# Optimization experiments

Hardware: AMD Instinct MI355X
Metric: run time of the kernel (lower is better)

The kernel has to match this reference:

```python
import jax, jax.numpy as jnp
import numpy as np

DIM, HEADS, DIM_HEAD = 1024, 16, 64
DIM_INNER = HEADS * DIM_HEAD  # 1024
SCALE = DIM_HEAD ** -0.5


def _rope(t):
    # t: [b, h, n, d]; interleaved-pair RoPE (lucidrains rotary-embedding-torch default)
    d = t.shape[-1]
    n = t.shape[-2]
    inv_freq = 1.0 / (10000.0 ** (jnp.arange(0, d, 2, dtype=jnp.float32) / d))
    angles = jnp.arange(n, dtype=jnp.float32)[:, None] * inv_freq[None, :]  # [n, d/2]
    cos, sin = jnp.cos(angles), jnp.sin(angles)
    t1, t2 = t[..., 0::2], t[..., 1::2]
    r1 = t1 * cos - t2 * sin
    r2 = t1 * sin + t2 * cos
    return jnp.stack([r1, r2], axis=-1).reshape(t.shape)


def setup_inputs() -> dict:
    key = jax.random.key(0)
    ks = jax.random.split(key, 8)
    b, n = 2, 2048
    inp = {
        "x": jax.random.normal(ks[0], (b, n, DIM), dtype=jnp.float32),
        "value_residual": jax.random.normal(ks[1], (b, HEADS, n, DIM_HEAD), dtype=jnp.float32),
        "gamma": jnp.ones((DIM,), dtype=jnp.float32),
        "w_qkv": jax.random.normal(ks[2], (DIM, 3 * DIM_INNER), dtype=jnp.float32) * (DIM ** -0.5),
        "w_mix": jax.random.normal(ks[3], (DIM, HEADS), dtype=jnp.float32) * (DIM ** -0.5),
        "b_mix": jnp.zeros((HEADS,), dtype=jnp.float32),
        "w_gates": jax.random.normal(ks[4], (DIM, HEADS), dtype=jnp.float32) * (DIM ** -0.5),
        "b_gates": jnp.zeros((HEADS,), dtype=jnp.float32),
        "w_out": jax.random.normal(ks[5], (DIM_INNER, DIM), dtype=jnp.float32) * (DIM_INNER ** -0.5),
    }
    return inp


def reference(x, value_residual, gamma, w_qkv, w_mix, b_mix, w_gates, b_gates, w_out):
    b, n, _ = x.shape
    # RMSNorm (lucidrains style: F.normalize * sqrt(dim) * gamma)
    norm = jnp.sqrt(jnp.sum(x * x, axis=-1, keepdims=True))
    xn = x / jnp.maximum(norm, 1e-12) * (DIM ** 0.5) * gamma

    qkv = xn @ w_qkv  # [b, n, 3*h*d]
    qkv = qkv.reshape(b, n, 3, HEADS, DIM_HEAD)
    q, k, v = [jnp.transpose(qkv[:, :, i], (0, 2, 1, 3)) for i in range(3)]  # [b,h,n,d]
    original_values = v

    # learned value-residual lerp
    mix = jax.nn.sigmoid(xn @ w_mix + b_mix)            # [b, n, h]
    mix = jnp.transpose(mix, (0, 2, 1))[..., None]       # [b, h, n, 1]
    v = v * (1.0 - mix) + value_residual * mix

    # rotary on q, k
    q = _rope(q)
    k = _rope(k)

    scores = jnp.einsum("bhid,bhjd->bhij", q, k) * SCALE
    attn = jax.nn.softmax(scores, axis=-1)
    out = jnp.einsum("bhij,bhjd->bhid", attn, v)         # [b, h, n, d]

    gates = jax.nn.sigmoid(xn @ w_gates + b_gates)       # [b, n, h]
    out = out * jnp.transpose(gates, (0, 2, 1))[..., None]

    out = jnp.transpose(out, (0, 2, 1, 3)).reshape(b, n, DIM_INNER)
    return out @ w_out, original_values
```

## Files before the change

### kernel.cpp

```cpp
#include <hip/hip_runtime.h>
#include <hip/hip_bf16.h>
#include <math.h>

#define DIMSZ 1024
#define HEADS 16
#define DHEAD 64
#define NSEQ  2048
#define BATCH 2
#define ROWS  (BATCH*NSEQ)
#define SCALE 0.125f
#define LOG2E 1.4426950408889634f

typedef __attribute__((ext_vector_type(8))) short short8;
typedef __attribute__((ext_vector_type(4))) float floatx4;
typedef __attribute__((ext_vector_type(16))) float floatx16;
typedef __attribute__((ext_vector_type(4))) unsigned uintx4;

#define MFMA16(a,b,c) __builtin_amdgcn_mfma_f32_16x16x32_bf16(a,b,c,0,0,0)
#define MFMA32(a,b,c) __builtin_amdgcn_mfma_f32_32x32x16_bf16(a,b,c,0,0,0)

__device__ __forceinline__ void gl2lds16(const void* g, void* l) {
    __builtin_amdgcn_global_load_lds(
        (const __attribute__((address_space(1))) unsigned int*)g,
        (__attribute__((address_space(3))) unsigned int*)l, 16, 0, 0);
}

__device__ __forceinline__ unsigned short bf16r(float a) {
    unsigned u = __float_as_uint(a);
    u += 0x7fff + ((u >> 16) & 1);
    return (unsigned short)(u >> 16);
}
__device__ __forceinline__ unsigned pack_bf16(float a, float b) {
    unsigned ua = __float_as_uint(a), ub = __float_as_uint(b);
    ua += 0x7fff + ((ua >> 16) & 1);
    ub += 0x7fff + ((ub >> 16) & 1);
    return (ua >> 16) | (ub & 0xffff0000u);
}
__device__ __forceinline__ float2 bf2f(unsigned u) {
    float2 r;
    r.x = __uint_as_float(u << 16);
    r.y = __uint_as_float(u & 0xffff0000u);
    return r;
}
__device__ __forceinline__ unsigned cvtpk(float lo, float hi) {
    unsigned r;
    asm("v_cvt_pk_bf16_f32 %0, %1, %2" : "=v"(r) : "v"(lo), "v"(hi));
    return r;
}
__device__ __forceinline__ void pl32swap(unsigned &a, unsigned &b) {
#if __has_builtin(__builtin_amdgcn_permlane32_swap)
    auto r = __builtin_amdgcn_permlane32_swap(a, b, false, false);
    a = (unsigned)r[0]; b = (unsigned)r[1];
#else
    asm volatile("v_permlane32_swap_b32 %0, %1" : "+v"(a), "+v"(b));
#endif
}
__device__ __forceinline__ float fexp2(float x) {
#if __has_builtin(__builtin_amdgcn_exp2f)
    return __builtin_amdgcn_exp2f(x);
#else
    return exp2f(x);
#endif
}
__device__ __forceinline__ float fsin_rev(float x) {
#if __has_builtin(__builtin_amdgcn_sinf)
    return __builtin_amdgcn_sinf(x);
#else
    return __sinf(x * 6.28318530717958647692f);
#endif
}
__device__ __forceinline__ float fcos_rev(float x) {
#if __has_builtin(__builtin_amdgcn_cosf)
    return __builtin_amdgcn_cosf(x);
#else
    return __cosf(x * 6.28318530717958647692f);
#endif
}

__global__ __launch_bounds__(256) void transpose_all_kernel(
    const float* __restrict__ w_qkv, const float* __restrict__ w_out,
    const float* __restrict__ w_mix, const float* __restrict__ w_gates,
    unsigned short* __restrict__ wqkvT, unsigned short* __restrict__ woutT,
    unsigned short* __restrict__ wmgT)
{
    __shared__ float t[32][33];
    const int tx = threadIdx.x & 31, tyy = threadIdx.x >> 5;
    const int bx = blockIdx.x;
    const int k0 = blockIdx.y * 32;
    if (bx < 128) {
        const float* src;
        unsigned short* dst;
        int N, n0;
        if (bx < 96) { src = w_qkv; dst = wqkvT; N = 3*DIMSZ; n0 = bx*32; }
        else         { src = w_out; dst = woutT; N = DIMSZ;   n0 = (bx-96)*32; }
        #pragma unroll
        for (int i = 0; i < 4; i++)
            t[tyy*4 + i][tx] = src[(size_t)(k0 + tyy*4 + i)*N + n0 + tx];
        __syncthreads();
        #pragma unroll
        for (int i = 0; i < 4; i++)
            dst[(size_t)(n0 + tyy*4 + i)*DIMSZ + k0 + tx] = bf16r(t[tx][tyy*4 + i]);
    } else {
        #pragma unroll
        for (int i = 0; i < 4; i++) {
            const int kk = k0 + tyy*4 + i;
            t[tyy*4 + i][tx] = (tx < 16) ? w_mix[kk*16 + tx]
                                         : w_gates[kk*16 + (tx - 16)];
        }
        __syncthreads();
        #pragma unroll
        for (int i = 0; i < 4; i++)
            wmgT[(size_t)(tyy*4 + i)*DIMSZ + k0 + tx] = bf16r(t[tx][tyy*4 + i]);
    }
}

__global__ __launch_bounds__(256) void rmsnorm_kernel(
    const float* __restrict__ x, const float* __restrict__ gamma,
    unsigned short* __restrict__ xnb)
{
    const int row = blockIdx.x;
    const int tid = threadIdx.x;
    __shared__ float wred[4];

    const float4 xv = ((const float4*)(x + (size_t)row * DIMSZ))[tid];
    float ss = xv.x*xv.x + xv.y*xv.y + xv.z*xv.z + xv.w*xv.w;
    #pragma unroll
    for (int off = 1; off < 64; off <<= 1) ss += __shfl_xor(ss, off);
    if ((tid & 63) == 0) wred[tid >> 6] = ss;
    __syncthreads();
    const float total = wred[0] + wred[1] + wred[2] + wred[3];
    const float inv = 32.0f / fmaxf(sqrtf(total), 1e-12f);
    const float4 gv = ((const float4*)gamma)[tid];
    uint2 pk;
    pk.x = pack_bf16(xv.x * inv * gv.x, xv.y * inv * gv.y);
    pk.y = pack_bf16(xv.z * inv * gv.z, xv.w * inv * gv.w);
    ((uint2*)(xnb + (size_t)row * DIMSZ))[tid] = pk;
}

__global__ __launch_bounds__(256) void mix_gates_mfma(
    const unsigned short* __restrict__ A, const unsigned short* __restrict__ WG,
    const float* __restrict__ b_mix, const float* __restrict__ b_gates,
    float* __restrict__ mixo, float* __restrict__ gateso)
{
    __shared__ short As[128*32];
    __shared__ short Bs[32*32];
    const int tid = threadIdx.x;
    const int wv = tid >> 6, lane = tid & 63;
    const int g = lane >> 4, c = lane & 15;
    const int bm = blockIdx.x * 128;

    floatx4 acc[2][2];
    #pragma unroll
    for (int mt = 0; mt < 2; mt++)
        #pragma unroll
        for (int nt = 0; nt < 2; nt++) acc[mt][nt] = (floatx4){0.f,0.f,0.f,0.f};

    for (int k0 = 0; k0 < DIMSZ; k0 += 32) {
        __syncthreads();
        #pragma unroll
        for (int r = 0; r < 2; r++) {
            const int ch = tid + 256*r;
            const int row = ch >> 2, cc = ch & 3;
            gl2lds16(A + (size_t)(bm + row)*DIMSZ + k0 + cc*8, (void*)(As + ch*8));
        }
        if (tid < 128)
            gl2lds16(WG + (size_t)(tid >> 2)*DIMSZ + k0 + (tid & 3)*8, (void*)(Bs + tid*8));
        __syncthreads();
        short8 af[2], bf[2];
        #pragma unroll
        for (int mt = 0; mt < 2; mt++) af[mt] = *(const short8*)(As + (wv*32 + mt*16 + c)*32 + g*8);
        #pragma unroll
        for (int nt = 0; nt < 2; nt++) bf[nt] = *(const short8*)(Bs + (nt*16 + c)*32 + g*8);
        #pragma unroll
        for (int mt = 0; mt < 2; mt++)
            #pragma unroll
            for (int nt = 0; nt < 2; nt++)
                acc[mt][nt] = MFMA16(af[mt], bf[nt], acc[mt][nt]);
    }
    const float bm_c = b_mix[c], bg_c = b_gates[c];
    #pragma unroll
    for (int mt = 0; mt < 2; mt++)
        #pragma unroll
        for (int r2 = 0; r2 < 4; r2++) {
            const int row = bm + wv*32 + mt*16 + g*4 + r2;
            const float lm = acc[mt][0][r2] + bm_c;
            const float lg = acc[mt][1][r2] + bg_c;
            mixo[(size_t)row*HEADS + c]   = 1.0f / (1.0f + fexp2(-lm * LOG2E));
            gateso[(size_t)row*HEADS + c] = 1.0f / (1.0f + fexp2(-lg * LOG2E));
        }
}

__global__ __launch_bounds__(256) void gemm_qkv_mfma(
    const unsigned short* __restrict__ A, const unsigned short* __restrict__ BT,
    unsigned short* __restrict__ qb, unsigned short* __restrict__ kb,
    float* __restrict__ vb)
{
    __shared__ short As[2][128*32];
    __shared__ short Bs[2][128*32];
    const int tid = threadIdx.x;
    const int wv = tid >> 6, lane = tid & 63;
    const int g = lane >> 4, c = lane & 15;
    const int wm = wv >> 1, wn = wv & 1;

    const int id = blockIdx.y * gridDim.x + blockIdx.x;
    const int xcd = id & 7, j = id >> 3;
    const int bnb = (xcd & 1)*12 + (j % 12);
    const int byb = (xcd >> 1)*8 + (j / 12);
    const int bm = byb * 128, bn = bnb * 128;

    floatx4 acc[4][4];
    #pragma unroll
    for (int mt = 0; mt < 4; mt++)
        #pragma unroll
        for (int nt = 0; nt < 4; nt++) acc[mt][nt] = (floatx4){0.f,0.f,0.f,0.f};

    const int srow = tid >> 2, scc = tid & 3;
    #pragma unroll
    for (int r = 0; r < 2; r++) {
        const int ch = tid + 256*r;
        const int row = ch >> 2, cc = ch & 3;
        gl2lds16(A  + (size_t)(bm + row)*DIMSZ + cc*8, (void*)(&As[0][0] + ch*8));
        gl2lds16(BT + (size_t)(bn + row)*DIMSZ + cc*8, (void*)(&Bs[0][0] + ch*8));
    }
    __syncthreads();

    for (int k0 = 0; k0 < DIMSZ; k0 += 32) {
        const int cur = (k0 >> 5) & 1;
        if (k0 + 32 < DIMSZ) {
            #pragma unroll
            for (int r = 0; r < 2; r++) {
                const int ch = tid + 256*r;
                const int row = ch >> 2, cc = ch & 3;
                gl2lds16(A  + (size_t)(bm + row)*DIMSZ + k0 + 32 + cc*8, (void*)(&As[cur^1][0] + ch*8));
                gl2lds16(BT + (size_t)(bn + row)*DIMSZ + k0 + 32 + cc*8, (void*)(&Bs[cur^1][0] + ch*8));
            }
        }
        short8 af[4], bf[4];
        #pragma unroll
        for (int mt = 0; mt < 4; mt++) af[mt] = *(const short8*)(&As[cur][0] + (wm*64 + mt*16 + c)*32 + g*8);
        #pragma unroll
        for (int nt = 0; nt < 4; nt++) bf[nt] = *(const short8*)(&Bs[cur][0] + (wn*64 + nt*16 + c)*32 + g*8);
        __builtin_amdgcn_s_setprio(1);
        #pragma unroll
        for (int mt = 0; mt < 4; mt++)
            #pragma unroll
            for (int nt = 0; nt < 4; nt++)
                acc[mt][nt] = MFMA16(af[mt], bf[nt], acc[mt][nt]);
        __builtin_amdgcn_s_setprio(0);
        __syncthreads();
    }
    (void)srow; (void)scc;

    const int i3 = bn >> 10;
    const int nb = bn - (i3 << 10);
    if (i3 < 2) {
        unsigned short* dst = (i3 == 0) ? qb : kb;
        short* wbuf = &As[0][0] + wv*1152;
        const int rd_row = lane >> 2, seg = lane & 3;
        #pragma unroll
        for (int mt = 0; mt < 4; mt++) {
            #pragma unroll
            for (int nt = 0; nt < 4; nt++)
                #pragma unroll
                for (int r2 = 0; r2 < 4; r2++)
                    wbuf[(g*4 + r2)*72 + nt*16 + c] = (short)bf16r(acc[mt][nt][r2]);
            __builtin_amdgcn_s_waitcnt(0xc07f);
            const uint4 v0 = *(const uint4*)&wbuf[rd_row*72 + seg*16];
            const uint4 v1 = *(const uint4*)&wbuf[rd_row*72 + seg*16 + 8];
            const int row = bm + wm*64 + mt*16 + rd_row;
            const int col = nb + wn*64 + seg*16;
            const int hh = col >> 6, dd = col & 63;
            const int bb2 = row >> 11, pos = row & 2047;
            unsigned short* dp = dst + (((size_t)(bb2*HEADS + hh)*NSEQ) + pos)*DHEAD + dd;
            *(uint4*)dp = v0;
            *(uint4*)(dp + 8) = v1;
            __builtin_amdgcn_s_waitcnt(0xc07f);
        }
    } else {
        #pragma unroll
        for (int mt = 0; mt < 4; mt++)
            #pragma unroll
            for (int nt = 0; nt < 4; nt++)
                #pragma unroll
                for (int r2 = 0; r2 < 4; r2++) {
                    const int row = bm + wm*64 + mt*16 + g*4 + r2;
                    const int col = nb + wn*64 + nt*16 + c;
                    const int hh = col >> 6, dd = col & 63;
                    const int bb2 = row >> 11, pos = row & 2047;
                    vb[(((size_t)(bb2*HEADS + hh)*NSEQ) + pos)*DHEAD + dd] = acc[mt][nt][r2];
                }
    }
}

__global__ __launch_bounds__(256) void rope_blend_kernel2(
    unsigned short* __restrict__ q, unsigned short* __restrict__ k,
    const float* __restrict__ vorig, const float* __restrict__ vres,
    const float* __restrict__ mixb, unsigned short* __restrict__ vT)
{
    __shared__ unsigned short vt[64*72];
    const int tid = threadIdx.x;
    const int bh = blockIdx.y, bb = bh >> 4, h = bh & 15;
    const int p0 = blockIdx.x * 64;
    {
        const int pr = tid >> 2, d0 = (tid & 3) * 16;
        const int pos = p0 + pr;
        const size_t base = ((size_t)bh*NSEQ + pos)*DHEAD + d0;

        uint4 qr0 = *(uint4*)(q + base), qr1 = *(uint4*)(q + base + 8);
        uint4 kr0 = *(uint4*)(k + base), kr1 = *(uint4*)(k + base + 8);
        unsigned qw[8] = {qr0.x, qr0.y, qr0.z, qr0.w, qr1.x, qr1.y, qr1.z, qr1.w};
        unsigned kw[8] = {kr0.x, kr0.y, kr0.z, kr0.w, kr1.x, kr1.y, kr1.z, kr1.w};
        const float QSC = SCALE * LOG2E;
        const float posf = (float)pos;
        #pragma unroll
        for (int j = 0; j < 8; j++) {
            const float pf = (float)((d0 >> 1) + j);
            const float rev = posf * fexp2(-pf * 0.41524101186092029f
                                           - 2.6514961294723187f);
            const float rf = rev - floorf(rev);
            const float sn = fsin_rev(rf);
            const float cs = fcos_rev(rf);
            float2 qv = bf2f(qw[j]);
            float2 kv = bf2f(kw[j]);
            const float q1 = qv.x*cs - qv.y*sn, q2 = qv.x*sn + qv.y*cs;
            const float k1 = kv.x*cs - kv.y*sn, k2 = kv.x*sn + kv.y*cs;
            qw[j] = pack_bf16(q1*QSC, q2*QSC);
            kw[j] = pack_bf16(k1, k2);
        }
        *(uint4*)(q + base)     = *(uint4*)(qw + 0);
        *(uint4*)(q + base + 8) = *(uint4*)(qw + 4);
        *(uint4*)(k + base)     = *(uint4*)(kw + 0);
        *(uint4*)(k + base + 8) = *(uint4*)(kw + 4);

        float vv[16], vr[16];
        #pragma unroll
        for (int i = 0; i < 4; i++) {
            *(float4*)(vv + i*4) = *(const float4*)(vorig + base + i*4);
            *(float4*)(vr + i*4) = *(const float4*)(vres + base + i*4);
        }
        const float mx = mixb[((size_t)(bb*NSEQ + pos))*HEADS + h];
        #pragma unroll
        for (int j = 0; j < 8; j++) {
            const float b0 = vv[2*j]*(1.f-mx)   + vr[2*j]*mx;
            const float b1 = vv[2*j+1]*(1.f-mx) + vr[2*j+1]*mx;
            vt[pr*72 + d0 + 2*j]     = bf16r(b0);
            vt[pr*72 + d0 + 2*j + 1] = bf16r(b1);
        }
    }
    __syncthreads();
    {
        const int dd = tid >> 2, c0 = (tid & 3) * 16;
        unsigned o[8];
        #pragma unroll
        for (int j = 0; j < 8; j++) {
            const unsigned a  = vt[(c0 + 2*j)*72 + dd];
            const unsigned b2 = vt[(c0 + 2*j + 1)*72 + dd];
            o[j] = a | (b2 << 16);
        }
        unsigned short* dst = vT + ((size_t)bh*DHEAD + dd)*NSEQ + p0 + c0;
        *(uint4*)(dst)     = *(uint4*)(o + 0);
        *(uint4*)(dst + 8) = *(uint4*)(o + 4);
    }
}

__global__ __launch_bounds__(256, 4) void attn_mfma_kernel(
    const unsigned short* __restrict__ qg,
    const unsigned short* __restrict__ kg,
    const unsigned short* __restrict__ vT,
    unsigned short* __restrict__ Op0,
    unsigned short* __restrict__ Op1,
    float* __restrict__ lpart)
{
    __shared__ short Kt[2][64*64];
    __shared__ short Vt[2][64*64];

    const int tid = threadIdx.x;
    const int w = tid >> 6, lane = tid & 63;
    const int hi = lane >> 5, cq = lane & 31;

    int wg = blockIdx.y * gridDim.x + blockIdx.x;
    wg = (wg & 7) * 128 + (wg >> 3);
    const int q0 = (wg & 15) * 128;
    const int byy = wg >> 4;
    const int bh = byy >> 1, s = byy & 1;
    const int bb = bh >> 4, h = bh & 15;

    short8 qf[4];
    #pragma unroll
    for (int kd = 0; kd < 4; kd++)
        qf[kd] = *(const short8*)(qg + ((size_t)bh*NSEQ + q0 + w*32 + cq)*DHEAD + kd*16 + hi*8);

    floatx16 O0{}, O1{};
    float lsum = 0.f;

    const unsigned short* kbase = kg + (size_t)bh*NSEQ*DHEAD;
    const unsigned short* vbase = vT + (size_t)bh*DHEAD*NSEQ;

    {
        const int kt = s*16;
        #pragma unroll
        for (int r = 0; r < 2; r++) {
            const int ch = tid + 256*r;
            const int row = ch >> 3;
            const int u = (ch & 7) ^ (row & 7);
            gl2lds16(kbase + (size_t)(kt*64 + row)*DHEAD + u*8, (void*)(&Kt[0][0] + ch*8));
            gl2lds16(vbase + (size_t)row*NSEQ + kt*64 + u*8,   (void*)(&Vt[0][0] + ch*8));
        }
    }
    __syncthreads();

    for (int i = 0; i < 16; i++) {
        const int cur = i & 1;
        const short* Ktc = &Kt[cur][0];
        const short* Vtc = &Vt[cur][0];

        if (i < 15) {
            const int kt = s*16 + i + 1;
            short* Ktn = &Kt[cur ^ 1][0];
            short* Vtn = &Vt[cur ^ 1][0];
            #pragma unroll
            for (int r = 0; r < 2; r++) {
                const int ch = tid + 256*r;
                const int row = ch >> 3;
                const int u = (ch & 7) ^ (row & 7);
                gl2lds16(kbase + (size_t)(kt*64 + row)*DHEAD + u*8, (void*)(Ktn + ch*8));
                gl2lds16(vbase + (size_t)row*NSEQ + kt*64 + u*8,   (void*)(Vtn + ch*8));
            }
        }

        #pragma unroll
        for (int kt2 = 0; kt2 < 2; kt2++) {
            floatx16 accS{};
            const int rowk = kt2*32 + cq;
            __builtin_amdgcn_s_setprio(1);
            #pragma unroll
            for (int kd = 0; kd < 4; kd++) {
                short8 kf = *(const short8*)(Ktc + rowk*64 + (((kd*2 + hi) ^ (cq & 7)) * 8));
                accS = MFMA32(kf, qf[kd], accS);
            }
            __builtin_amdgcn_s_setprio(0);

            float p[16];
            #pragma unroll
            for (int r = 0; r < 16; r++) p[r] = fexp2(accS[r]);
            const float a1 = (p[0]+p[1]) + (p[2]+p[3]);
            const float a2 = (p[4]+p[5]) + (p[6]+p[7]);
            const float a3 = (p[8]+p[9]) + (p[10]+p[11]);
            const float a4 = (p[12]+p[13]) + (p[14]+p[15]);
            lsum += (a1+a2) + (a3+a4);

            unsigned d0 = cvtpk(p[0],  p[1]);
            unsigned d1 = cvtpk(p[2],  p[3]);
            unsigned d2 = cvtpk(p[4],  p[5]);
            unsigned d3 = cvtpk(p[6],  p[7]);
            unsigned d4 = cvtpk(p[8],  p[9]);
            unsigned d5 = cvtpk(p[10], p[11]);
            unsigned d6 = cvtpk(p[12], p[13]);
            unsigned d7 = cvtpk(p[14], p[15]);
            pl32swap(d0, d2);
            pl32swap(d1, d3);
            pl32swap(d4, d6);
            pl32swap(d5, d7);
            const uintx4 t0 = {d0, d1, d2, d3};
            const uintx4 t1 = {d4, d5, d6, d7};
            const short8 pf0 = __builtin_bit_cast(short8, t0);
            const short8 pf1 = __builtin_bit_cast(short8, t1);

            __builtin_amdgcn_s_setprio(1);
            #pragma unroll
            for (int ks2 = 0; ks2 < 2; ks2++) {
                const short8 pf = ks2 ? pf1 : pf0;
                #pragma unroll
                for (int nt2 = 0; nt2 < 2; nt2++) {
                    const int rv = nt2*32 + cq;
                    short8 vf = *(const short8*)(Vtc + rv*64 + (((kt2*4 + ks2*2 + hi) ^ (cq & 7)) * 8));
                    if (nt2 == 0) O0 = MFMA32(pf, vf, O0);
                    else          O1 = MFMA32(pf, vf, O1);
                }
            }
            __builtin_amdgcn_s_setprio(0);
        }
        __syncthreads();
    }

    unsigned short* Op = s ? Op1 : Op0;
    float l = lsum + __shfl_xor(lsum, 32);
    if (hi == 0)
        lpart[((size_t)s*ROWS + bb*NSEQ + q0 + w*32 + cq)*HEADS + h] = l;
    #pragma unroll
    for (int reg = 0; reg < 16; reg++) {
        const int qq = (reg & 3) + 8*(reg >> 2) + 4*hi;
        const int rowg = q0 + w*32 + qq;
        unsigned short* op = Op + ((size_t)(bb*NSEQ + rowg))*DIMSZ + h*DHEAD + cq;
        op[0]  = bf16r(O0[reg]);
        op[32] = bf16r(O1[reg]);
    }
}

__global__ __launch_bounds__(256) void attn_combine_kernel(
    const unsigned short* __restrict__ Op1, const float* __restrict__ lpart,
    const float* __restrict__ gates, unsigned short* __restrict__ attnO)
{
    const int idx = blockIdx.x * 256 + threadIdx.x;
    const int row = idx >> 7;
    const int c8 = (idx & 127) * 8;
    const int h = c8 >> 6;
    const float l0 = lpart[(size_t)row*HEADS + h];
    const float l1 = lpart[((size_t)ROWS + row)*HEADS + h];
    const float gt = gates[(size_t)row*HEADS + h];
    const float sc = gt / (l0 + l1);
    const size_t base = (size_t)row*DIMSZ + c8;
    const uint4 a = *(const uint4*)(attnO + base);
    const uint4 b = *(const uint4*)(Op1 + base);
    const unsigned aw[4] = {a.x, a.y, a.z, a.w};
    const unsigned bw[4] = {b.x, b.y, b.z, b.w};
    unsigned o[4];
    #pragma unroll
    for (int j = 0; j < 4; j++) {
        const float2 fa = bf2f(aw[j]);
        const float2 fb = bf2f(bw[j]);
        o[j] = pack_bf16((fa.x + fb.x)*sc, (fa.y + fb.y)*sc);
    }
    *(uint4*)(attnO + base) = *(uint4*)o;
}

__global__ __launch_bounds__(256) void gemm_out_mfma(
    const unsigned short* __restrict__ A, const unsigned short* __restrict__ BT,
    float* __restrict__ out0)
{
    __shared__ short As[2][128*32];
    __shared__ short Bs[2][64*32];
    const int tid = threadIdx.x;
    const int wv = tid >> 6, lane = tid & 63;
    const int g = lane >> 4, c = lane & 15;
    const int wm = wv >> 1, wn = wv & 1;

    const int id = blockIdx.y * gridDim.x + blockIdx.x;
    const int xcd = id & 7, j = id >> 3;
    const int bnb = j & 15, byb = xcd*4 + (j >> 4);
    const int bm = byb * 128, bn = bnb * 64;

    floatx4 acc[4][2];
    #pragma unroll
    for (int mt = 0; mt < 4; mt++)
        #pragma unroll
        for (int nt = 0; nt < 2; nt++) acc[mt][nt] = (floatx4){0.f,0.f,0.f,0.f};

    #pragma unroll
    for (int r = 0; r < 2; r++) {
        const int ch = tid + 256*r;
        const int row = ch >> 2, cc = ch & 3;
        gl2lds16(A + (size_t)(bm + row)*DIMSZ + cc*8, (void*)(&As[0][0] + ch*8));
    }
    gl2lds16(BT + (size_t)(bn + (tid >> 2))*DIMSZ + (tid & 3)*8, (void*)(&Bs[0][0] + tid*8));
    __syncthreads();

    for (int k0 = 0; k0 < DIMSZ; k0 += 32) {
        const int cur = (k0 >> 5) & 1;
        if (k0 + 32 < DIMSZ) {
            #pragma unroll
            for (int r = 0; r < 2; r++) {
                const int ch = tid + 256*r;
                const int row = ch >> 2, cc = ch & 3;
                gl2lds16(A + (size_t)(bm + row)*DIMSZ + k0 + 32 + cc*8, (void*)(&As[cur^1][0] + ch*8));
            }
            gl2lds16(BT + (size_t)(bn + (tid >> 2))*DIMSZ + k0 + 32 + (tid & 3)*8, (void*)(&Bs[cur^1][0] + tid*8));
        }
        short8 af[4], bf[2];
        #pragma unroll
        for (int mt = 0; mt < 4; mt++) af[mt] = *(const short8*)(&As[cur][0] + (wm*64 + mt*16 + c)*32 + g*8);
        #pragma unroll
        for (int nt = 0; nt < 2; nt++) bf[nt] = *(const short8*)(&Bs[cur][0] + (wn*32 + nt*16 + c)*32 + g*8);
        __builtin_amdgcn_s_setprio(1);
        #pragma unroll
        for (int mt = 0; mt < 4; mt++)
            #pragma unroll
            for (int nt = 0; nt < 2; nt++)
                acc[mt][nt] = MFMA16(af[mt], bf[nt], acc[mt][nt]);
        __builtin_amdgcn_s_setprio(0);
        __syncthreads();
    }
    #pragma unroll
    for (int mt = 0; mt < 4; mt++)
        #pragma unroll
        for (int nt = 0; nt < 2; nt++)
            #pragma unroll
            for (int r2 = 0; r2 < 4; r2++) {
                const int row = bm + wm*64 + mt*16 + g*4 + r2;
                const int col = bn + wn*32 + nt*16 + c;
                out0[(size_t)row*DIMSZ + col] = acc[mt][nt][r2];
            }
}

extern "C" void kernel_launch(void* const* d_in, const int* in_sizes, int n_in,
                              void* d_out, int out_size, void* d_ws, size_t ws_size,
                              hipStream_t stream) {
    const float* x       = (const float*)d_in[0];
    const float* vres    = (const float*)d_in[1];
    const float* gamma   = (const float*)d_in[2];
    const float* w_qkv   = (const float*)d_in[3];
    const float* w_mix   = (const float*)d_in[4];
    const float* b_mix   = (const float*)d_in[5];
    const float* w_gates = (const float*)d_in[6];
    const float* b_gates = (const float*)d_in[7];
    const float* w_out   = (const float*)d_in[8];

    float* out0 = (float*)d_out;
    float* out1 = out0 + (size_t)ROWS * DIMSZ;

    char* ws = (char*)d_ws;
    unsigned short* xnb   = (unsigned short*)(ws);
    unsigned short* wqkvT = (unsigned short*)(ws + (8u<<20));
    unsigned short* woutT = (unsigned short*)(ws + (14u<<20));
    unsigned short* qb2   = (unsigned short*)(ws + (16u<<20));
    unsigned short* kb2   = (unsigned short*)(ws + (24u<<20));
    unsigned short* vT    = (unsigned short*)(ws + (32u<<20));
    unsigned short* attnO = (unsigned short*)(ws + (40u<<20));
    float*          mixb  = (float*)(ws + (48u<<20));
    float*          gatesb= (float*)(ws + (48u<<20) + 262144);
    unsigned short* wmgT  = (unsigned short*)(ws + (49u<<20));
    unsigned short* Op1   = (unsigned short*)(ws + (50u<<20));
    float*          lpart = (float*)(ws + (58u<<20));

    transpose_all_kernel<<<dim3(129, DIMSZ/32), 256, 0, stream>>>(
        w_qkv, w_out, w_mix, w_gates, wqkvT, woutT, wmgT);

    rmsnorm_kernel<<<ROWS, 256, 0, stream>>>(x, gamma, xnb);

    mix_gates_mfma<<<ROWS/128, 256, 0, stream>>>(
        xnb, wmgT, b_mix, b_gates, mixb, gatesb);

    gemm_qkv_mfma<<<dim3(3*DIMSZ/128, ROWS/128), 256, 0, stream>>>(
        xnb, wqkvT, qb2, kb2, out1);

    rope_blend_kernel2<<<dim3(NSEQ/64, BATCH*HEADS), 256, 0, stream>>>(
        qb2, kb2, out1, vres, mixb, vT);

    attn_mfma_kernel<<<dim3(NSEQ/128, BATCH*HEADS*2), 256, 0, stream>>>(
        qb2, kb2, vT, attnO, Op1, lpart);

    attn_combine_kernel<<<ROWS*DIMSZ/8/256, 256, 0, stream>>>(
        Op1, lpart, gatesb, attnO);

    gemm_out_mfma<<<dim3(DIMSZ/64, ROWS/128), 256, 0, stream>>>(
        attnO, woutT, out0);
}
```

Baseline: 234.9 us.

## Triple-buffer GEMM staging, compute softmax rowsum via MFMA, tweak LDS swizzle

Both the QKV and output GEMMs move from double to triple-buffered LDS staging, with explicit vmcnt waits and raw barriers so two tiles of global loads stay in flight. The attention kernel drops the scalar exp-sum reduction and instead accumulates the row sum with an extra MFMA against a ones vector. The K/V LDS swizzle also changes to XOR in bit 3 of the row. These changes trade more LDS and an extra MFMA per step for fewer VALU adds, less barrier stall, and possibly fewer bank conflicts.

```diff
diff --git a/kernel.cpp b/kernel.cpp
--- a/kernel.cpp
+++ b/kernel.cpp
@@ -76,6 +76,8 @@
     return __cosf(x * 6.28318530717958647692f);
 #endif
 }
+
+#define SWZ(row) (((row) & 7) ^ (((row) >> 3) & 1))
 
 __global__ __launch_bounds__(256) void transpose_all_kernel(
     const float* __restrict__ w_qkv, const float* __restrict__ w_out,
@@ -190,13 +192,26 @@
         }
 }
 
+__device__ __forceinline__ void stage_qkv(
+    const unsigned short* A, const unsigned short* BT,
+    short* as, short* bs, int bm, int bn, int kk, int tid)
+{
+    #pragma unroll
+    for (int r = 0; r < 2; r++) {
+        const int ch = tid + 256*r;
+        const int row = ch >> 2, j = ch & 3;
+        gl2lds16(A  + (size_t)(bm + row)*DIMSZ + kk + j*8, (void*)(as + ch*8));
+        gl2lds16(BT + (size_t)(bn + row)*DIMSZ + kk + j*8, (void*)(bs + ch*8));
+    }
+}
+
 __global__ __launch_bounds__(256) void gemm_qkv_mfma(
     const unsigned short* __restrict__ A, const unsigned short* __restrict__ BT,
     unsigned short* __restrict__ qb, unsigned short* __restrict__ kb,
     float* __restrict__ vb)
 {
-    __shared__ short As[2][128*32];
-    __shared__ short Bs[2][128*32];
+    __shared__ short As[3][128*32];
+    __shared__ short Bs[3][128*32];
     const int tid = threadIdx.x;
     const int wv = tid >> 6, lane = tid & 63;
     const int g = lane >> 4, c = lane & 15;
@@ -214,27 +229,18 @@
         #pragma unroll
         for (int nt = 0; nt < 4; nt++) acc[mt][nt] = (floatx4){0.f,0.f,0.f,0.f};
 
-    const int srow = tid >> 2, scc = tid & 3;
-    #pragma unroll
-    for (int r = 0; r < 2; r++) {
-        const int ch = tid + 256*r;
-        const int row = ch >> 2, cc = ch & 3;
-        gl2lds16(A  + (size_t)(bm + row)*DIMSZ + cc*8, (void*)(&As[0][0] + ch*8));
-        gl2lds16(BT + (size_t)(bn + row)*DIMSZ + cc*8, (void*)(&Bs[0][0] + ch*8));
-    }
-    __syncthreads();
-
-    for (int k0 = 0; k0 < DIMSZ; k0 += 32) {
-        const int cur = (k0 >> 5) & 1;
-        if (k0 + 32 < DIMSZ) {
-            #pragma unroll
-            for (int r = 0; r < 2; r++) {
-                const int ch = tid + 256*r;
-                const int row = ch >> 2, cc = ch & 3;
-                gl2lds16(A  + (size_t)(bm + row)*DIMSZ + k0 + 32 + cc*8, (void*)(&As[cur^1][0] + ch*8));
-                gl2lds16(BT + (size_t)(bn + row)*DIMSZ + k0 + 32 + cc*8, (void*)(&Bs[cur^1][0] + ch*8));
-            }
-        }
+    stage_qkv(A, BT, &As[0][0], &Bs[0][0], bm, bn, 0,  tid);
+    stage_qkv(A, BT, &As[1][0], &Bs[1][0], bm, bn, 32, tid);
+    asm volatile("s_waitcnt vmcnt(4)" ::: "memory");
+    __builtin_amdgcn_s_barrier();
+    __builtin_amdgcn_sched_barrier(0);
+
+    int cur = 0, nxt = 2;
+    for (int i = 0; i < 32; i++) {
+        const int k0 = i*32;
+        if (i < 30)
+            stage_qkv(A, BT, &As[nxt][0], &Bs[nxt][0], bm, bn, k0 + 64, tid);
+
         short8 af[4], bf[4];
         #pragma unroll
         for (int mt = 0; mt < 4; mt++) af[mt] = *(const short8*)(&As[cur][0] + (wm*64 + mt*16 + c)*32 + g*8);
@@ -247,9 +253,17 @@
             for (int nt = 0; nt < 4; nt++)
                 acc[mt][nt] = MFMA16(af[mt], bf[nt], acc[mt][nt]);
         __builtin_amdgcn_s_setprio(0);
-        __syncthreads();
-    }
-    (void)srow; (void)scc;
+
+        if (i < 31) {
+            if (i < 30) asm volatile("s_waitcnt vmcnt(4)" ::: "memory");
+            else        asm volatile("s_waitcnt vmcnt(0)" ::: "memory");
+            __builtin_amdgcn_s_barrier();
+            __builtin_amdgcn_sched_barrier(0);
+        }
+        cur = (cur == 2) ? 0 : cur + 1;
+        nxt = (nxt == 2) ? 0 : nxt + 1;
+    }
+    __syncthreads();
 
     const int i3 = bn >> 10;
     const int nb = bn - (i3 << 10);
@@ -390,8 +404,11 @@
     for (int kd = 0; kd < 4; kd++)
         qf[kd] = *(const short8*)(qg + ((size_t)bh*NSEQ + q0 + w*32 + cq)*DHEAD + kd*16 + hi*8);
 
-    floatx16 O0{}, O1{};
-    float lsum = 0.f;
+    short8 onesb;
+    #pragma unroll
+    for (int j = 0; j < 8; j++) onesb[j] = (short)0x3F80;
+
+    floatx16 O0{}, O1{}, Ol{};
 
     const unsigned short* kbase = kg + (size_t)bh*NSEQ*DHEAD;
     const unsigned short* vbase = vT + (size_t)bh*DHEAD*NSEQ;
@@ -402,7 +419,7 @@
         for (int r = 0; r < 2; r++) {
             const int ch = tid + 256*r;
             const int row = ch >> 3;
-            const int u = (ch & 7) ^ (row & 7);
+            const int u = (ch & 7) ^ SWZ(row);
             gl2lds16(kbase + (size_t)(kt*64 + row)*DHEAD + u*8, (void*)(&Kt[0][0] + ch*8));
             gl2lds16(vbase + (size_t)row*NSEQ + kt*64 + u*8,   (void*)(&Vt[0][0] + ch*8));
         }
@@ -422,7 +439,7 @@
             for (int r = 0; r < 2; r++) {
                 const int ch = tid + 256*r;
                 const int row = ch >> 3;
-                const int u = (ch & 7) ^ (row & 7);
+                const int u = (ch & 7) ^ SWZ(row);
                 gl2lds16(kbase + (size_t)(kt*64 + row)*DHEAD + u*8, (void*)(Ktn + ch*8));
                 gl2lds16(vbase + (size_t)row*NSEQ + kt*64 + u*8,   (void*)(Vtn + ch*8));
             }
@@ -435,7 +452,7 @@
             __builtin_amdgcn_s_setprio(1);
             #pragma unroll
             for (int kd = 0; kd < 4; kd++) {
-                short8 kf = *(const short8*)(Ktc + rowk*64 + (((kd*2 + hi) ^ (cq & 7)) * 8));
+                short8 kf = *(const short8*)(Ktc + rowk*64 + (((kd*2 + hi) ^ SWZ(rowk)) * 8));
                 accS = MFMA32(kf, qf[kd], accS);
             }
             __builtin_amdgcn_s_setprio(0);
@@ -443,11 +460,6 @@
             float p[16];
             #pragma unroll
             for (int r = 0; r < 16; r++) p[r] = fexp2(accS[r]);
-            const float a1 = (p[0]+p[1]) + (p[2]+p[3]);
-            const float a2 = (p[4]+p[5]) + (p[6]+p[7]);
-            const float a3 = (p[8]+p[9]) + (p[10]+p[11]);
-            const float a4 = (p[12]+p[13]) + (p[14]+p[15]);
-            lsum += (a1+a2) + (a3+a4);
 
             unsigned d0 = cvtpk(p[0],  p[1]);
             unsigned d1 = cvtpk(p[2],  p[3]);
@@ -473,10 +485,11 @@
                 #pragma unroll
                 for (int nt2 = 0; nt2 < 2; nt2++) {
                     const int rv = nt2*32 + cq;
-                    short8 vf = *(const short8*)(Vtc + rv*64 + (((kt2*4 + ks2*2 + hi) ^ (cq & 7)) * 8));
+                    short8 vf = *(const short8*)(Vtc + rv*64 + (((kt2*4 + ks2*2 + hi) ^ SWZ(rv)) * 8));
                     if (nt2 == 0) O0 = MFMA32(pf, vf, O0);
                     else          O1 = MFMA32(pf, vf, O1);
                 }
+                Ol = MFMA32(pf, onesb, Ol);
             }
             __builtin_amdgcn_s_setprio(0);
         }
@@ -484,9 +497,13 @@
     }
 
     unsigned short* Op = s ? Op1 : Op0;
-    float l = lsum + __shfl_xor(lsum, 32);
-    if (hi == 0)
-        lpart[((size_t)s*ROWS + bb*NSEQ + q0 + w*32 + cq)*HEADS + h] = l;
+    if (cq == 0) {
+        #pragma unroll
+        for (int reg = 0; reg < 16; reg++) {
+            const int qq = (reg & 3) + 8*(reg >> 2) + 4*hi;
+            lpart[((size_t)s*ROWS + bb*NSEQ + q0 + w*32 + qq)*HEADS + h] = Ol[reg];
+        }
+    }
     #pragma unroll
     for (int reg = 0; reg < 16; reg++) {
         const int qq = (reg & 3) + 8*(reg >> 2) + 4*hi;
@@ -524,12 +541,25 @@
     *(uint4*)(attnO + base) = *(uint4*)o;
 }
 
+__device__ __forceinline__ void stage_out(
+    const unsigned short* A, const unsigned short* BT,
+    short* as, short* bs, int bm, int bn, int kk, int tid)
+{
+    #pragma unroll
+    for (int r = 0; r < 2; r++) {
+        const int ch = tid + 256*r;
+        const int row = ch >> 2, j = ch & 3;
+        gl2lds16(A + (size_t)(bm + row)*DIMSZ + kk + j*8, (void*)(as + ch*8));
+    }
+    gl2lds16(BT + (size_t)(bn + (tid >> 2))*DIMSZ + kk + (tid & 3)*8, (void*)(bs + tid*8));
+}
+
 __global__ __launch_bounds__(256) void gemm_out_mfma(
     const unsigned short* __restrict__ A, const unsigned short* __restrict__ BT,
     float* __restrict__ out0)
 {
-    __shared__ short As[2][128*32];
-    __shared__ short Bs[2][64*32];
+    __shared__ short As[3][128*32];
+    __shared__ short Bs[3][64*32];
     const int tid = threadIdx.x;
     const int wv = tid >> 6, lane = tid & 63;
     const int g = lane >> 4, c = lane & 15;
@@ -546,26 +576,18 @@
         #pragma unroll
         for (int nt = 0; nt < 2; nt++) acc[mt][nt] = (floatx4){0.f,0.f,0.f,0.f};
 
-    #pragma unroll
-    for (int r = 0; r < 2; r++) {
-        const int ch = tid + 256*r;
-        const int row = ch >> 2, cc = ch & 3;
-        gl2lds16(A + (size_t)(bm + row)*DIMSZ + cc*8, (void*)(&As[0][0] + ch*8));
-    }
-    gl2lds16(BT + (size_t)(bn + (tid >> 2))*DIMSZ + (tid & 3)*8, (void*)(&Bs[0][0] + tid*8));
-    __syncthreads();
-
-    for (int k0 = 0; k0 < DIMSZ; k0 += 32) {
-        const int cur = (k0 >> 5) & 1;
-        if (k0 + 32 < DIMSZ) {
-            #pragma unroll
-            for (int r = 0; r < 2; r++) {
-                const int ch = tid + 256*r;
-                const int row = ch >> 2, cc = ch & 3;
-                gl2lds16(A + (size_t)(bm + row)*DIMSZ + k0 + 32 + cc*8, (void*)(&As[cur^1][0] + ch*8));
-            }
-            gl2lds16(BT + (size_t)(bn + (tid >> 2))*DIMSZ + k0 + 32 + (tid & 3)*8, (void*)(&Bs[cur^1][0] + tid*8));
-        }
+    stage_out(A, BT, &As[0][0], &Bs[0][0], bm, bn, 0,  tid);
+    stage_out(A, BT, &As[1][0], &Bs[1][0], bm, bn, 32, tid);
+    asm volatile("s_waitcnt vmcnt(3)" ::: "memory");
+    __builtin_amdgcn_s_barrier();
+    __builtin_amdgcn_sched_barrier(0);
+
+    int cur = 0, nxt = 2;
+    for (int i = 0; i < 32; i++) {
+        const int k0 = i*32;
+        if (i < 30)
+            stage_out(A, BT, &As[nxt][0], &Bs[nxt][0], bm, bn, k0 + 64, tid);
+
         short8 af[4], bf[2];
         #pragma unroll
         for (int mt = 0; mt < 4; mt++) af[mt] = *(const short8*)(&As[cur][0] + (wm*64 + mt*16 + c)*32 + g*8);
@@ -578,8 +600,17 @@
             for (int nt = 0; nt < 2; nt++)
                 acc[mt][nt] = MFMA16(af[mt], bf[nt], acc[mt][nt]);
         __builtin_amdgcn_s_setprio(0);
-        __syncthreads();
-    }
+
+        if (i < 31) {
+            if (i < 30) asm volatile("s_waitcnt vmcnt(3)" ::: "memory");
+            else        asm volatile("s_waitcnt vmcnt(0)" ::: "memory");
+            __builtin_amdgcn_s_barrier();
+            __builtin_amdgcn_sched_barrier(0);
+        }
+        cur = (cur == 2) ? 0 : cur + 1;
+        nxt = (nxt == 2) ? 0 : nxt + 1;
+    }
+
     #pragma unroll
     for (int mt = 0; mt < 4; mt++)
         #pragma unroll
```

Result: no change. 233.7 us (-0.5%).
